# Kernel optimization log

Hardware: AMD Instinct MI355X
Metric: run time of the kernel (lower is better)

The kernel has to match this reference:

```python
import jax, jax.numpy as jnp
import numpy as np

N = 8192
K = 64
EPS = 1e-7
BN_EPS = 1e-5


def _norm(x):
    return jnp.sqrt(jnp.sum(x * x, axis=-1, keepdims=True))


def _bn(x, gamma, beta):
    # BatchNorm2d in training mode (batch statistics, biased variance)
    mu = jnp.mean(x, axis=(0, 2, 3), keepdims=True)
    var = jnp.mean((x - mu) ** 2, axis=(0, 2, 3), keepdims=True)
    return gamma.reshape(1, -1, 1, 1) * (x - mu) / jnp.sqrt(var + BN_EPS) + beta.reshape(1, -1, 1, 1)


def _conv1x1(x, w, b):
    # 1x1 conv == per-pixel linear: x [B,C,H,W], w [O,C]
    return jnp.einsum('bchw,oc->bohw', x, w) + b.reshape(1, -1, 1, 1)


def setup_inputs() -> dict:
    key = jax.random.key(0)
    ks = jax.random.split(key, 24)
    d = {}
    d['points'] = jax.random.normal(ks[0], (1, N, 3), jnp.float32)
    # graph_conv weights (torch code re-draws these every forward; here fixed params)
    lim0 = float(np.sqrt(6.0 / (4 + 64)))
    d['gw0'] = jax.random.uniform(ks[1], (4, 64), jnp.float32, -lim0, lim0)
    lim = float(np.sqrt(6.0 / (64 + 64)))
    for i in range(1, 5):
        d[f'gw{i}'] = jax.random.uniform(ks[1 + i], (64, 64), jnp.float32, -lim, lim)
    # mlp_1: 4->64->128, mlp_2: 192->256->1024 (1x1 convs + BN)
    d['c1w'] = jax.random.normal(ks[6], (64, 4), jnp.float32) * 0.1
    d['c1b'] = jnp.zeros((64,), jnp.float32)
    d['bn1g'] = jnp.ones((64,), jnp.float32)
    d['bn1b'] = jnp.zeros((64,), jnp.float32)
    d['c2w'] = jax.random.normal(ks[7], (128, 64), jnp.float32) * 0.1
    d['c2b'] = jnp.zeros((128,), jnp.float32)
    d['bn2g'] = jnp.ones((128,), jnp.float32)
    d['bn2b'] = jnp.zeros((128,), jnp.float32)
    d['c3w'] = jax.random.normal(ks[8], (256, 192), jnp.float32) * 0.05
    d['c3b'] = jnp.zeros((256,), jnp.float32)
    d['bn3g'] = jnp.ones((256,), jnp.float32)
    d['bn3b'] = jnp.zeros((256,), jnp.float32)
    d['c4w'] = jax.random.normal(ks[9], (1024, 256), jnp.float32) * 0.05
    d['c4b'] = jnp.zeros((1024,), jnp.float32)
    d['bn4g'] = jnp.ones((1024,), jnp.float32)
    d['bn4b'] = jnp.zeros((1024,), jnp.float32)
    return d


def _knn_search(points, k):
    # pairwise squared distances via ||a||^2 - 2ab + ||b||^2
    r = jnp.sum(points * points, axis=-1, keepdims=True)          # [1,N,1]
    dis = r - 2.0 * jnp.einsum('bnd,bmd->bnm', points, points) + jnp.swapaxes(r, 1, 2)
    _, idx = jax.lax.top_k(-dis, k)                                # [1,N,K]
    knn_pts = jax.vmap(lambda p, i: p[i])(points, idx)             # [1,N,K,3]
    return knn_pts


def _proj_knn(knn_pts):
    b, n, k, _ = knn_pts.shape
    pc = knn_pts - knn_pts[:, :, :1, :]                            # center on first neighbor (self)
    vn = jnp.sqrt(jnp.sum(pc * pc, axis=-1))                       # [1,N,K]
    id1 = jnp.argmax(vn, axis=-1)                                  # farthest neighbor
    a1 = jnp.take_along_axis(pc, jnp.broadcast_to(id1[:, :, None, None], (b, n, 1, 3)), axis=2)[:, :, 0, :]
    a1 = a1 / (_norm(a1) + EPS)
    a2 = jnp.mean(pc, axis=2)
    a2 = a2 / (_norm(a2) + EPS)
    a3 = a1 + 1.5 * a2
    a3 = a3 / (_norm(a3) + EPS)
    den = _norm(pc) + EPS                                          # [1,N,K,1]
    f1 = jnp.sum(pc * a1[:, :, None, :], axis=-1, keepdims=True) / den
    f2 = jnp.sum(pc * a2[:, :, None, :], axis=-1, keepdims=True) / den
    f3 = jnp.sum(pc * a3[:, :, None, :], axis=-1, keepdims=True) / den
    return jnp.concatenate([f1, f2, f3, vn[..., None]], axis=-1)   # [1,N,K,4]


def _proj_points(points):
    b, n, _ = points.shape
    vn = jnp.sqrt(jnp.sum(points * points, axis=-1))               # [1,N]
    i1 = jnp.argmax(vn, axis=-1)
    i2 = jnp.argmin(vn, axis=-1)
    a1 = jnp.take_along_axis(points, jnp.broadcast_to(i1[:, None, None], (b, 1, 3)), axis=1)[:, 0, :]
    a1 = a1 / (_norm(a1) + EPS)
    a2 = jnp.take_along_axis(points, jnp.broadcast_to(i2[:, None, None], (b, 1, 3)), axis=1)[:, 0, :]
    a2 = a2 / (_norm(a2) + EPS)
    a3 = a1 + 1.5 * a2
    a3 = a3 / (_norm(a3) + EPS)
    den = _norm(points) + EPS                                      # [1,N,1]
    f1 = jnp.sum(points * a1[:, None, :], axis=-1, keepdims=True) / den
    f2 = jnp.sum(points * a2[:, None, :], axis=-1, keepdims=True) / den
    f3 = jnp.sum(points * a3[:, None, :], axis=-1, keepdims=True) / den
    return jnp.concatenate([f1, f2, f3, vn[..., None]], axis=-1)   # [1,N,4]


def reference(points, gw0, gw1, gw2, gw3, gw4,
              c1w, c1b, bn1g, bn1b, c2w, c2b, bn2g, bn2b,
              c3w, c3b, bn3g, bn3b, c4w, c4b, bn4g, bn4b):
    n = points.shape[1]
    # upper branch: KNN -> rotation-invariant local feats -> 5-layer MLP -> max over K
    knn_pts = _knn_search(points, K)
    feat_up = _proj_knn(knn_pts)                                   # [1,N,K,4]
    x = feat_up.reshape(-1, 4)
    for w in (gw0, gw1, gw2, gw3, gw4):
        x = jax.nn.relu(x @ w)
    x = x.reshape(1, n, K, 64)
    emb_up = jnp.max(x, axis=2, keepdims=True)                     # [1,N,1,64]
    emb_up = emb_up.reshape(1, 64, n, 1)                           # raw view (reshape), as in torch
    # lower branch: global rotation-invariant feats -> mlp_1
    feat_down = _proj_points(points)                               # [1,N,4]
    emb_down = feat_down.reshape(1, 4, n, 1)                       # raw view (reshape), as in torch
    h = jax.nn.relu(_bn(_conv1x1(emb_down, c1w, c1b), bn1g, bn1b))
    h = jax.nn.relu(_bn(_conv1x1(h, c2w, c2b), bn2g, bn2b))        # [1,128,N,1]
    emb = jnp.concatenate([emb_up, h], axis=1)                     # [1,192,N,1]
    out = jax.nn.relu(_bn(_conv1x1(emb, c3w, c3b), bn3g, bn3b))
    out = jax.nn.relu(_bn(_conv1x1(out, c4w, c4b), bn4g, bn4b))    # [1,1024,N,1]
    return out
```

## Files before the change

kernel.cpp:

```cpp
#include <hip/hip_runtime.h>
#include <hip/hip_bf16.h>

#define NPTS 8192
#define KNN 64
#define EPSF 1e-7f

#define OFF_P4      0
#define OFF_STATS   32768
#define OFF_AVEC    36000
#define OFF_PART    36012
#define OFF_FEATDN  36864
#define OFF_WT1     69632
#define OFF_GWT     69888
#define OFF_BW2     79104
#define OFF_BW3     83200
#define OFF_BW4     107776
#define OFF_XB1     238848
#define OFF_XB3     500992
#define OFF_XB4     1287424
#define OFF_Y1      2336000
#define OFF_Y2      2860288
#define OFF_Y3      3908864
#define OFF_FEATUP  6006016

typedef __bf16 bf16x8 __attribute__((ext_vector_type(8)));
typedef float  f32x4  __attribute__((ext_vector_type(4)));

__device__ __forceinline__ unsigned f2u(float f) {
    unsigned u = __float_as_uint(f);
    return ((int)u >= 0) ? (u | 0x80000000u) : ~u;
}
__device__ __forceinline__ float key_to_f(unsigned long long k) {
    unsigned v = (unsigned)(k >> 32);
    unsigned ob = (v & 0x80000000u) ? (v ^ 0x80000000u) : ~v;
    return __uint_as_float(ob);
}
__device__ __forceinline__ unsigned short f2bf(float x) {
    unsigned u = __float_as_uint(x);
    unsigned r = (u + 0x7FFFu + ((u >> 16) & 1u)) >> 16;
    return (unsigned short)r;
}
__device__ __forceinline__ unsigned long long u64min(unsigned long long a, unsigned long long b){ return a < b ? a : b; }
__device__ __forceinline__ unsigned long long u64max(unsigned long long a, unsigned long long b){ return a < b ? b : a; }

__device__ __forceinline__ unsigned long long sort_merge(
    unsigned long long key, unsigned long long cur, int lane)
{
    #pragma unroll
    for (int k = 2; k <= 64; k <<= 1) {
        #pragma unroll
        for (int j = k >> 1; j > 0; j >>= 1) {
            unsigned long long o = __shfl_xor(key, j);
            bool up = ((lane & k) == 0);
            bool lower = ((lane & j) == 0);
            key = (lower == up) ? u64min(key, o) : u64max(key, o);
        }
    }
    unsigned long long rev = __shfl(key, 63 - lane);
    unsigned long long m = u64min(cur, rev);
    #pragma unroll
    for (int j = 32; j > 0; j >>= 1) {
        unsigned long long o = __shfl_xor(m, j);
        m = ((lane & j) == 0) ? u64min(m, o) : u64max(m, o);
    }
    return m;
}

__global__ __launch_bounds__(256) void prep_a_kernel(
    const float* __restrict__ points, float* __restrict__ ws)
{
    const int n = blockIdx.x * 256 + threadIdx.x;
    float x = points[3*n+0], y = points[3*n+1], z = points[3*n+2];
    float rr = x*x + y*y + z*z;
    ((float4*)(ws + OFF_P4))[n] = make_float4(x, y, z, rr);
    float vn = sqrtf(rr);
    unsigned b = __float_as_uint(vn);
    unsigned long long mxk = ((unsigned long long)b << 32) | (unsigned long long)(0xFFFFFFFFu - (unsigned)n);
    unsigned long long mnk = ((unsigned long long)b << 32) | (unsigned long long)(unsigned)n;
    for (int j = 32; j > 0; j >>= 1) {
        mxk = u64max(mxk, __shfl_xor(mxk, j));
        mnk = u64min(mnk, __shfl_xor(mnk, j));
    }
    __shared__ unsigned long long smx[4], smn[4];
    int wid = threadIdx.x >> 6;
    if ((threadIdx.x & 63) == 0) { smx[wid] = mxk; smn[wid] = mnk; }
    __syncthreads();
    if (threadIdx.x == 0) {
        unsigned long long MX = 0ull, MN = ~0ull;
        for (int i = 0; i < 4; ++i) { MX = u64max(MX, smx[i]); MN = u64min(MN, smn[i]); }
        unsigned long long* parts = (unsigned long long*)(ws + OFF_PART);
        parts[2*blockIdx.x + 0] = MX;
        parts[2*blockIdx.x + 1] = MN;
    }
}

__global__ __launch_bounds__(64) void prep_b_kernel(
    const float* __restrict__ points, float* __restrict__ ws)
{
    const int lane = threadIdx.x;
    const unsigned long long* parts = (const unsigned long long*)(ws + OFF_PART);
    unsigned long long mxk = (lane < 32) ? parts[2*lane + 0] : 0ull;
    unsigned long long mnk = (lane < 32) ? parts[2*lane + 1] : ~0ull;
    for (int j = 32; j > 0; j >>= 1) {
        mxk = u64max(mxk, __shfl_xor(mxk, j));
        mnk = u64min(mnk, __shfl_xor(mnk, j));
    }
    if (lane == 0) {
        int i1 = (int)(0xFFFFFFFFu - (unsigned)(mxk & 0xFFFFFFFFu));
        int i2 = (int)(unsigned)(mnk & 0xFFFFFFFFu);
        float a1x = points[3*i1+0], a1y = points[3*i1+1], a1z = points[3*i1+2];
        float n1 = sqrtf(a1x*a1x + a1y*a1y + a1z*a1z) + EPSF;
        a1x /= n1; a1y /= n1; a1z /= n1;
        float a2x = points[3*i2+0], a2y = points[3*i2+1], a2z = points[3*i2+2];
        float n2 = sqrtf(a2x*a2x + a2y*a2y + a2z*a2z) + EPSF;
        a2x /= n2; a2y /= n2; a2z /= n2;
        float a3x = a1x + 1.5f*a2x, a3y = a1y + 1.5f*a2y, a3z = a1z + 1.5f*a2z;
        float n3 = sqrtf(a3x*a3x + a3y*a3y + a3z*a3z) + EPSF;
        a3x /= n3; a3y /= n3; a3z /= n3;
        float* av = ws + OFF_AVEC;
        av[0]=a1x; av[1]=a1y; av[2]=a1z;
        av[3]=a2x; av[4]=a2y; av[5]=a2z;
        av[6]=a3x; av[7]=a3y; av[8]=a3z;
    }
}

__global__ __launch_bounds__(256) void prep_c_kernel(float* __restrict__ ws)
{
    const int n = blockIdx.x * 256 + threadIdx.x;
    const float* av = ws + OFF_AVEC;
    float4 v = ((const float4*)(ws + OFF_P4))[n];
    float vn = sqrtf(v.w);
    float den = vn + EPSF;
    float f1 = (v.x*av[0] + v.y*av[1] + v.z*av[2]) / den;
    float f2 = (v.x*av[3] + v.y*av[4] + v.z*av[5]) / den;
    float f3 = (v.x*av[6] + v.y*av[7] + v.z*av[8]) / den;
    float4* f4 = (float4*)(ws + OFF_FEATDN + 4*n);
    *f4 = make_float4(f1, f2, f3, vn);
}

__global__ __launch_bounds__(256) void wt_kernel(
    const float* __restrict__ c1w, const float* __restrict__ c2w,
    const float* __restrict__ c3w, const float* __restrict__ c4w,
    const float* __restrict__ gw0, const float* __restrict__ gw1,
    const float* __restrict__ gw2, const float* __restrict__ gw3,
    const float* __restrict__ gw4,
    float* __restrict__ ws)
{
    const int t = blockIdx.x * 256 + threadIdx.x;
    const int T = gridDim.x * 256;
    for (int m = t; m < 2944; m += T) ws[OFF_STATS + m] = 0.f;
    for (int m = t; m < 64*4; m += T) { int o = m >> 2, c = m & 3; ws[OFF_WT1 + c*64 + o] = c1w[m]; }

    unsigned short* bw2 = (unsigned short*)(ws + OFF_BW2);
    for (int m = t; m < 128*64; m += T)   bw2[m] = f2bf(c2w[m]);
    unsigned short* bw3 = (unsigned short*)(ws + OFF_BW3);
    for (int m = t; m < 256*192; m += T)  bw3[m] = f2bf(c3w[m]);
    unsigned short* bw4 = (unsigned short*)(ws + OFF_BW4);
    for (int m = t; m < 1024*256; m += T) bw4[m] = f2bf(c4w[m]);

    unsigned short* gwt = (unsigned short*)(ws + OFF_GWT);
    for (int m = t; m < 2048; m += T) {
        int o = m >> 5, i = m & 31;
        gwt[m] = (i < 4) ? f2bf(gw0[i*64 + o]) : (unsigned short)0;
    }
    const float* gsrc[4] = {gw1, gw2, gw3, gw4};
    for (int l = 0; l < 4; ++l) {
        const float* g = gsrc[l];
        unsigned short* dst = gwt + 2048 + l*4096;
        for (int m = t; m < 4096; m += T) { int o = m >> 6, i = m & 63; dst[m] = f2bf(g[i*64 + o]); }
    }
}

__global__ __launch_bounds__(512) void knn_feat_kernel(
    const float4* __restrict__ p4, float4* __restrict__ feat_up)
{
    __shared__ __align__(16) float4 scand[2048];
    __shared__ unsigned long long queue[8][128];
    const int lane = threadIdx.x & 63;
    const int wid  = threadIdx.x >> 6;
    const int q = blockIdx.x * 8 + wid;

    const float4 qa = p4[q];
    unsigned long long cur = ~0ull;
    float kthd = __builtin_inff();
    int qc = 0;
    unsigned long long* Q = queue[wid];

    for (int base = 0; base < NPTS; base += 2048) {
        __syncthreads();
        for (int t = threadIdx.x; t < 2048; t += 512) scand[t] = p4[base + t];
        __syncthreads();
        #pragma unroll 2
        for (int sub = 0; sub < 2048; sub += 64) {
            float4 cd = scand[sub + lane];
            float dot = fmaf(qa.x, cd.x, fmaf(qa.y, cd.y, qa.z * cd.z));
            float d   = fmaf(-2.f, dot, qa.w) + cd.w;
            bool p = d < kthd;
            unsigned long long m = __ballot(p);
            if (m) {
                int prefix = __builtin_amdgcn_mbcnt_hi((unsigned)(m >> 32),
                              __builtin_amdgcn_mbcnt_lo((unsigned)m, 0));
                if (p) Q[qc + prefix] = ((unsigned long long)f2u(d) << 32)
                                      | (unsigned long long)(unsigned)(base + sub + lane);
                qc += __popcll(m);
                if (qc >= 64) {
                    qc -= 64;
                    cur = sort_merge(Q[qc + lane], cur, lane);
                    kthd = key_to_f(__shfl(cur, 63));
                }
            }
        }
    }
    cur = sort_merge((lane < qc) ? Q[lane] : ~0ull, cur, lane);

    int nidx = (int)(unsigned)(cur & 0xFFFFFFFFu);
    float4 np = p4[nidx];
    float ox = __shfl(np.x, 0), oy = __shfl(np.y, 0), oz = __shfl(np.z, 0);
    float pcx = np.x - ox, pcy = np.y - oy, pcz = np.z - oz;
    float vn = sqrtf(pcx*pcx + pcy*pcy + pcz*pcz);

    unsigned long long ak = ((unsigned long long)__float_as_uint(vn) << 32)
                          | (unsigned long long)(unsigned)(63 - lane);
    for (int s = 32; s > 0; s >>= 1) ak = u64max(ak, __shfl_xor(ak, s));
    int id1 = 63 - (int)(unsigned)(ak & 0xFFFFFFFFu);

    float a1x = __shfl(pcx, id1), a1y = __shfl(pcy, id1), a1z = __shfl(pcz, id1);
    float n1 = sqrtf(a1x*a1x + a1y*a1y + a1z*a1z) + EPSF;
    a1x /= n1; a1y /= n1; a1z /= n1;

    float sx = pcx, sy = pcy, sz = pcz;
    for (int s = 32; s > 0; s >>= 1) {
        sx += __shfl_xor(sx, s); sy += __shfl_xor(sy, s); sz += __shfl_xor(sz, s);
    }
    float a2x = sx * (1.f/64.f), a2y = sy * (1.f/64.f), a2z = sz * (1.f/64.f);
    float n2 = sqrtf(a2x*a2x + a2y*a2y + a2z*a2z) + EPSF;
    a2x /= n2; a2y /= n2; a2z /= n2;

    float a3x = a1x + 1.5f*a2x, a3y = a1y + 1.5f*a2y, a3z = a1z + 1.5f*a2z;
    float n3 = sqrtf(a3x*a3x + a3y*a3y + a3z*a3z) + EPSF;
    a3x /= n3; a3y /= n3; a3z /= n3;

    float den = vn + EPSF;
    float f1 = (pcx*a1x + pcy*a1y + pcz*a1z) / den;
    float f2 = (pcx*a2x + pcy*a2y + pcz*a2z) / den;
    float f3 = (pcx*a3x + pcy*a3y + pcz*a3z) / den;
    feat_up[q*64 + lane] = make_float4(f1, f2, f3, vn);
}

#define BROW 72
__global__ __launch_bounds__(256) void mlp_kernel(
    const float4* __restrict__ feat_up,
    const unsigned short* __restrict__ gwt,
    unsigned short* __restrict__ xb3)
{
    __shared__ __align__(16) unsigned short Blds[4][64 * BROW];
    const int lane = threadIdx.x & 63;
    const int wid  = threadIdx.x >> 6;
    const int q = blockIdx.x * 4 + wid;
    const int c = lane & 15, g = lane >> 4;
    unsigned short* B = Blds[wid];

    {
        float4 f = feat_up[q*64 + lane];
        uint2 p0;
        p0.x = (unsigned)f2bf(f.x) | ((unsigned)f2bf(f.y) << 16);
        p0.y = (unsigned)f2bf(f.z) | ((unsigned)f2bf(f.w) << 16);
        *(uint2*)&B[lane*BROW] = p0;
        *(uint2*)&B[lane*BROW + 4] = make_uint2(0, 0);
        uint4 z4 = make_uint4(0, 0, 0, 0);
        *(uint4*)&B[lane*BROW + 8]  = z4;
        *(uint4*)&B[lane*BROW + 16] = z4;
        *(uint4*)&B[lane*BROW + 24] = z4;
    }

    const unsigned short* Wl[5] = {gwt, gwt + 2048, gwt + 6144, gwt + 10240, gwt + 14336};
    f32x4 acc[4][4];

    for (int layer = 0; layer < 5; ++layer) {
        const int wstride = (layer == 0) ? 32 : 64;
        const int nks = (layer == 0) ? 1 : 2;
        #pragma unroll
        for (int mb = 0; mb < 4; ++mb)
            #pragma unroll
            for (int nb = 0; nb < 4; ++nb)
                acc[mb][nb] = (f32x4){0.f, 0.f, 0.f, 0.f};

        for (int ks = 0; ks < nks; ++ks) {
            bf16x8 af[4], bf[4];
            #pragma unroll
            for (int mb = 0; mb < 4; ++mb)
                af[mb] = *(const bf16x8*)(Wl[layer] + (mb*16 + c)*wstride + ks*32 + g*8);
            #pragma unroll
            for (int nb = 0; nb < 4; ++nb)
                bf[nb] = *(const bf16x8*)&B[(nb*16 + c)*BROW + ks*32 + g*8];
            #pragma unroll
            for (int mb = 0; mb < 4; ++mb)
                #pragma unroll
                for (int nb = 0; nb < 4; ++nb)
                    acc[mb][nb] = __builtin_amdgcn_mfma_f32_16x16x32_bf16(af[mb], bf[nb], acc[mb][nb], 0, 0, 0);
        }

        if (layer < 4) {
            #pragma unroll
            for (int mb = 0; mb < 4; ++mb) {
                #pragma unroll
                for (int nb = 0; nb < 4; ++nb) {
                    f32x4 a = acc[mb][nb];
                    float r0 = fmaxf(a[0], 0.f), r1 = fmaxf(a[1], 0.f);
                    float r2 = fmaxf(a[2], 0.f), r3 = fmaxf(a[3], 0.f);
                    uint2 pw;
                    pw.x = (unsigned)f2bf(r0) | ((unsigned)f2bf(r1) << 16);
                    pw.y = (unsigned)f2bf(r2) | ((unsigned)f2bf(r3) << 16);
                    *(uint2*)&B[(nb*16 + c)*BROW + mb*16 + g*4] = pw;
                }
            }
        }
    }

    const int cc = q >> 7;
    const int pbase = (q & 127) << 6;
    #pragma unroll
    for (int mb = 0; mb < 4; ++mb) {
        float v[4];
        #pragma unroll
        for (int r = 0; r < 4; ++r)
            v[r] = fmaxf(fmaxf(fmaxf(acc[mb][0][r], acc[mb][1][r]),
                               fmaxf(acc[mb][2][r], acc[mb][3][r])), 0.f);
        #pragma unroll
        for (int mask = 1; mask <= 8; mask <<= 1)
            #pragma unroll
            for (int r = 0; r < 4; ++r)
                v[r] = fmaxf(v[r], __shfl_xor(v[r], mask));
        if (c == 0) {
            #pragma unroll
            for (int r = 0; r < 4; ++r) {
                const int f = mb*16 + g*4 + r;
                xb3[(size_t)(pbase + f) * 192 + cc] = f2bf(v[r]);
            }
        }
    }
}

__global__ __launch_bounds__(256) void conv1_kernel(
    const float* __restrict__ x, const float* __restrict__ wt,
    const float* __restrict__ bias, float* __restrict__ y,
    float* __restrict__ stout)
{
    const int tid = threadIdx.x;
    const int p  = blockIdx.x * 256 + tid;
    const int o0 = blockIdx.y * 32;
    float acc[32];
    #pragma unroll
    for (int u = 0; u < 32; ++u) acc[u] = bias[o0 + u];
    #pragma unroll
    for (int c = 0; c < 4; ++c) {
        float xv = x[c * NPTS + p];
        const float* wr = wt + c * 64 + o0;
        #pragma unroll
        for (int u = 0; u < 32; ++u) acc[u] = fmaf(xv, wr[u], acc[u]);
    }
    #pragma unroll
    for (int u = 0; u < 32; ++u) y[(o0 + u) * NPTS + p] = acc[u];

    __shared__ float ps[4][32], pss[4][32];
    const int wid = tid >> 6, lane = tid & 63;
    #pragma unroll
    for (int u = 0; u < 32; ++u) {
        float s = acc[u], ss = acc[u] * acc[u];
        for (int j = 32; j > 0; j >>= 1) { s += __shfl_xor(s, j); ss += __shfl_xor(ss, j); }
        if (lane == 0) { ps[wid][u] = s; pss[wid][u] = ss; }
    }
    __syncthreads();
    if (tid < 32) {
        float S  = ps[0][tid] + ps[1][tid] + ps[2][tid] + ps[3][tid];
        float SS = pss[0][tid] + pss[1][tid] + pss[2][tid] + pss[3][tid];
        atomicAdd(&stout[o0 + tid], S);
        atomicAdd(&stout[64 + o0 + tid], SS);
    }
}

__global__ __launch_bounds__(256) void bnpack_kernel(
    const float* __restrict__ y, const float* __restrict__ st,
    const float* __restrict__ gam, const float* __restrict__ bet,
    int C, int stride, int coff, unsigned short* __restrict__ xb)
{
    __shared__ float sc[256], sh[256];
    __shared__ __align__(16) unsigned short tile[64][264];
    const int tid = threadIdx.x;
    for (int cc = tid; cc < C; cc += 256) {
        float mu  = st[cc] * (1.f / 8192.f);
        float var = st[C + cc] * (1.f / 8192.f) - mu * mu;
        float s = gam[cc] / sqrtf(var + 1e-5f);
        sc[cc] = s; sh[cc] = bet[cc] - mu * s;
    }
    __syncthreads();
    const int pl = tid & 63, g = tid >> 6;
    const int p = blockIdx.x * 64 + pl;
    for (int c0 = g * 8; c0 < C; c0 += 32) {
        unsigned pk[4];
        #pragma unroll
        for (int h = 0; h < 4; ++h) {
            float v0 = fmaxf(fmaf(y[(c0 + 2*h    ) * NPTS + p], sc[c0 + 2*h    ], sh[c0 + 2*h    ]), 0.f);
            float v1 = fmaxf(fmaf(y[(c0 + 2*h + 1) * NPTS + p], sc[c0 + 2*h + 1], sh[c0 + 2*h + 1]), 0.f);
            pk[h] = (unsigned)f2bf(v0) | ((unsigned)f2bf(v1) << 16);
        }
        *(uint4*)&tile[pl][c0] = make_uint4(pk[0], pk[1], pk[2], pk[3]);
    }
    __syncthreads();
    const int cpr = C >> 3;
    const int nch = 64 * cpr;
    for (int idx = tid; idx < nch; idx += 256) {
        int r = idx / cpr, cc = (idx - r * cpr) * 8;
        *(uint4*)&xb[(size_t)(blockIdx.x * 64 + r) * stride + coff + cc] = *(uint4*)&tile[r][cc];
    }
}

__global__ __launch_bounds__(256) void conv_mfma_kernel(
    const unsigned short* __restrict__ A, const unsigned short* __restrict__ Bx,
    const float* __restrict__ bias, int K, int M,
    float* __restrict__ y, float* __restrict__ stout)
{
    const int lane = threadIdx.x & 63;
    const int w = threadIdx.x >> 6;
    const int n0 = blockIdx.x * 256 + w * 64;
    const int m0 = blockIdx.y * 64;
    const int c = lane & 15, g = lane >> 4;

    f32x4 acc[4][4];
    #pragma unroll
    for (int mt = 0; mt < 4; ++mt)
        #pragma unroll
        for (int nt = 0; nt < 4; ++nt)
            acc[mt][nt] = (f32x4){0.f, 0.f, 0.f, 0.f};

    for (int k0 = 0; k0 < K; k0 += 32) {
        bf16x8 af[4], bf[4];
        #pragma unroll
        for (int mt = 0; mt < 4; ++mt)
            af[mt] = *(const bf16x8*)(A + (size_t)(m0 + mt*16 + c) * K + k0 + g*8);
        #pragma unroll
        for (int nt = 0; nt < 4; ++nt)
            bf[nt] = *(const bf16x8*)(Bx + (size_t)(n0 + nt*16 + c) * K + k0 + g*8);
        #pragma unroll
        for (int mt = 0; mt < 4; ++mt)
            #pragma unroll
            for (int nt = 0; nt < 4; ++nt)
                acc[mt][nt] = __builtin_amdgcn_mfma_f32_16x16x32_bf16(af[mt], bf[nt], acc[mt][nt], 0, 0, 0);
    }

    #pragma unroll
    for (int mt = 0; mt < 4; ++mt) {
        float s[4], ss[4];
        #pragma unroll
        for (int r = 0; r < 4; ++r) {
            const int o = m0 + mt*16 + g*4 + r;
            const float bv = bias[o];
            float sum = 0.f, sq = 0.f;
            #pragma unroll
            for (int nt = 0; nt < 4; ++nt) {
                float v = acc[mt][nt][r] + bv;
                y[(size_t)o * NPTS + n0 + nt*16 + c] = v;
                sum += v; sq += v * v;
            }
            s[r] = sum; ss[r] = sq;
        }
        #pragma unroll
        for (int mask = 1; mask <= 8; mask <<= 1)
            #pragma unroll
            for (int r = 0; r < 4; ++r) {
                s[r]  += __shfl_xor(s[r],  mask);
                ss[r] += __shfl_xor(ss[r], mask);
            }
        if (c == 0) {
            #pragma unroll
            for (int r = 0; r < 4; ++r) {
                const int o = m0 + mt*16 + g*4 + r;
                atomicAdd(&stout[o], s[r]);
                atomicAdd(&stout[M + o], ss[r]);
            }
        }
    }
}

__global__ __launch_bounds__(256) void bnrelu_kernel(
    const float4* y, const float* __restrict__ st,
    const float* __restrict__ g, const float* __restrict__ b,
    float4* out, int C)
{
    int idx = blockIdx.x * 256 + threadIdx.x;
    int c = idx >> 11;
    float mu  = st[c] * (1.f / 8192.f);
    float var = st[C + c] * (1.f / 8192.f) - mu * mu;
    float scale = g[c] / sqrtf(var + 1e-5f);
    float sh = b[c] - mu * scale;
    float4 v = y[idx];
    v.x = fmaxf(fmaf(v.x, scale, sh), 0.f);
    v.y = fmaxf(fmaf(v.y, scale, sh), 0.f);
    v.z = fmaxf(fmaf(v.z, scale, sh), 0.f);
    v.w = fmaxf(fmaf(v.w, scale, sh), 0.f);
    out[idx] = v;
}

extern "C" void kernel_launch(void* const* d_in, const int* in_sizes, int n_in,
                              void* d_out, int out_size, void* d_ws, size_t ws_size,
                              hipStream_t stream) {
    const float* points = (const float*)d_in[0];
    const float* gw0 = (const float*)d_in[1];
    const float* gw1 = (const float*)d_in[2];
    const float* gw2 = (const float*)d_in[3];
    const float* gw3 = (const float*)d_in[4];
    const float* gw4 = (const float*)d_in[5];
    const float* c1w = (const float*)d_in[6];  const float* c1b = (const float*)d_in[7];
    const float* bn1g = (const float*)d_in[8]; const float* bn1b = (const float*)d_in[9];
    const float* c2w = (const float*)d_in[10]; const float* c2b = (const float*)d_in[11];
    const float* bn2g = (const float*)d_in[12];const float* bn2b = (const float*)d_in[13];
    const float* c3w = (const float*)d_in[14]; const float* c3b = (const float*)d_in[15];
    const float* bn3g = (const float*)d_in[16];const float* bn3b = (const float*)d_in[17];
    const float* c4w = (const float*)d_in[18]; const float* c4b = (const float*)d_in[19];
    const float* bn4g = (const float*)d_in[20];const float* bn4b = (const float*)d_in[21];

    float* ws = (float*)d_ws;
    float* p4f    = ws + OFF_P4;
    float* featdn = ws + OFF_FEATDN;
    float* featup = ws + OFF_FEATUP;
    float* y1 = ws + OFF_Y1; float* y2 = ws + OFF_Y2; float* y3 = ws + OFF_Y3;
    float* s1 = ws + OFF_STATS + 0;
    float* s2 = ws + OFF_STATS + 128;
    float* s3 = ws + OFF_STATS + 384;
    float* s4 = ws + OFF_STATS + 896;
    float* wt1 = ws + OFF_WT1;
    const unsigned short* gwt = (const unsigned short*)(ws + OFF_GWT);
    const unsigned short* bw2 = (const unsigned short*)(ws + OFF_BW2);
    const unsigned short* bw3 = (const unsigned short*)(ws + OFF_BW3);
    const unsigned short* bw4 = (const unsigned short*)(ws + OFF_BW4);
    unsigned short* xb1 = (unsigned short*)(ws + OFF_XB1);
    unsigned short* xb3 = (unsigned short*)(ws + OFF_XB3);
    unsigned short* xb4 = (unsigned short*)(ws + OFF_XB4);
    float* outp = (float*)d_out;

    prep_a_kernel<<<32, 256, 0, stream>>>(points, ws);
    prep_b_kernel<<<1, 64, 0, stream>>>(points, ws);
    prep_c_kernel<<<32, 256, 0, stream>>>(ws);
    wt_kernel<<<256, 256, 0, stream>>>(c1w, c2w, c3w, c4w, gw0, gw1, gw2, gw3, gw4, ws);

    knn_feat_kernel<<<1024, 512, 0, stream>>>((const float4*)p4f, (float4*)featup);
    mlp_kernel<<<2048, 256, 0, stream>>>((const float4*)featup, gwt, xb3);

    conv1_kernel<<<dim3(32, 2), 256, 0, stream>>>(featdn, wt1, c1b, y1, s1);
    bnpack_kernel<<<128, 256, 0, stream>>>(y1, s1, bn1g, bn1b, 64, 64, 0, xb1);
    conv_mfma_kernel<<<dim3(32, 2), 256, 0, stream>>>(bw2, xb1, c2b, 64, 128, y2, s2);
    bnpack_kernel<<<128, 256, 0, stream>>>(y2, s2, bn2g, bn2b, 128, 192, 64, xb3);
    conv_mfma_kernel<<<dim3(32, 4), 256, 0, stream>>>(bw3, xb3, c3b, 192, 256, y3, s3);
    bnpack_kernel<<<128, 256, 0, stream>>>(y3, s3, bn3g, bn3b, 256, 256, 0, xb4);
    conv_mfma_kernel<<<dim3(32, 16), 256, 0, stream>>>(bw4, xb4, c4b, 256, 1024, outp, s4);
    bnrelu_kernel<<<8192, 256, 0, stream>>>((const float4*)outp, s4, bn4g, bn4b, (float4*)outp, 1024);
}
```

Measured before the change: 354.9 us.

## Merge prep kernels, drop constant distance term in KNN, use hardware bf16 convert

Folds the point-prep and weight-conversion kernels into one launch, and moves the axis-vector computation into prep_c so each block recomputes it into shared memory. Two kernel launches go away. The KNN scan now compares ||c||^2 - 2q·c, leaving out the per-query constant ||q||^2, which does not change the ranking. It also processes two 64-candidate groups per iteration to expose more ILP. The f2bf helper now uses a compiler bf16 cast instead of manual rounding, which is equivalent apart from possible NaN handling, and a packing helper is added.

Measured after the change: 350.0 us. No clear change (-1.4%).

```diff
diff --git a/kernel.cpp b/kernel.cpp
--- a/kernel.cpp
+++ b/kernel.cpp
@@ -7,7 +7,6 @@
 
 #define OFF_P4      0
 #define OFF_STATS   32768
-#define OFF_AVEC    36000
 #define OFF_PART    36012
 #define OFF_FEATDN  36864
 #define OFF_WT1     69632
@@ -36,9 +35,12 @@
     return __uint_as_float(ob);
 }
 __device__ __forceinline__ unsigned short f2bf(float x) {
-    unsigned u = __float_as_uint(x);
-    unsigned r = (u + 0x7FFFu + ((u >> 16) & 1u)) >> 16;
-    return (unsigned short)r;
+    union { __bf16 h; unsigned short s; } u;
+    u.h = (__bf16)x;
+    return u.s;
+}
+__device__ __forceinline__ unsigned packbf2(float lo, float hi) {
+    return (unsigned)f2bf(lo) | ((unsigned)f2bf(hi) << 16);
 }
 __device__ __forceinline__ unsigned long long u64min(unsigned long long a, unsigned long long b){ return a < b ? a : b; }
 __device__ __forceinline__ unsigned long long u64max(unsigned long long a, unsigned long long b){ return a < b ? b : a; }
@@ -66,68 +68,97 @@
     return m;
 }
 
-__global__ __launch_bounds__(256) void prep_a_kernel(
-    const float* __restrict__ points, float* __restrict__ ws)
-{
-    const int n = blockIdx.x * 256 + threadIdx.x;
-    float x = points[3*n+0], y = points[3*n+1], z = points[3*n+2];
-    float rr = x*x + y*y + z*z;
-    ((float4*)(ws + OFF_P4))[n] = make_float4(x, y, z, rr);
-    float vn = sqrtf(rr);
-    unsigned b = __float_as_uint(vn);
-    unsigned long long mxk = ((unsigned long long)b << 32) | (unsigned long long)(0xFFFFFFFFu - (unsigned)n);
-    unsigned long long mnk = ((unsigned long long)b << 32) | (unsigned long long)(unsigned)n;
-    for (int j = 32; j > 0; j >>= 1) {
-        mxk = u64max(mxk, __shfl_xor(mxk, j));
-        mnk = u64min(mnk, __shfl_xor(mnk, j));
-    }
-    __shared__ unsigned long long smx[4], smn[4];
-    int wid = threadIdx.x >> 6;
-    if ((threadIdx.x & 63) == 0) { smx[wid] = mxk; smn[wid] = mnk; }
+__global__ __launch_bounds__(256) void prepwt_kernel(
+    const float* __restrict__ points,
+    const float* __restrict__ c1w, const float* __restrict__ c2w,
+    const float* __restrict__ c3w, const float* __restrict__ c4w,
+    const float* __restrict__ gw0, const float* __restrict__ gw1,
+    const float* __restrict__ gw2, const float* __restrict__ gw3,
+    const float* __restrict__ gw4,
+    float* __restrict__ ws)
+{
+    const int t = blockIdx.x * 256 + threadIdx.x;
+    const int T = 256 * 256;
+    for (int m = t; m < 2944; m += T) ws[OFF_STATS + m] = 0.f;
+    for (int m = t; m < 64*4; m += T) { int o = m >> 2, c = m & 3; ws[OFF_WT1 + c*64 + o] = c1w[m]; }
+
+    unsigned short* bw2 = (unsigned short*)(ws + OFF_BW2);
+    for (int m = t; m < 128*64; m += T)   bw2[m] = f2bf(c2w[m]);
+    unsigned short* bw3 = (unsigned short*)(ws + OFF_BW3);
+    for (int m = t; m < 256*192; m += T)  bw3[m] = f2bf(c3w[m]);
+    unsigned short* bw4 = (unsigned short*)(ws + OFF_BW4);
+    for (int m = t; m < 1024*256; m += T) bw4[m] = f2bf(c4w[m]);
+
+    unsigned short* gwt = (unsigned short*)(ws + OFF_GWT);
+    for (int m = t; m < 2048; m += T) {
+        int o = m >> 5, i = m & 31;
+        gwt[m] = (i < 4) ? f2bf(gw0[i*64 + o]) : (unsigned short)0;
+    }
+    const float* gsrc[4] = {gw1, gw2, gw3, gw4};
+    for (int l = 0; l < 4; ++l) {
+        const float* g = gsrc[l];
+        unsigned short* dst = gwt + 2048 + l*4096;
+        for (int m = t; m < 4096; m += T) { int o = m >> 6, i = m & 63; dst[m] = f2bf(g[i*64 + o]); }
+    }
+
+    if (blockIdx.x < 32) {
+        const int n = blockIdx.x * 256 + threadIdx.x;
+        float x = points[3*n+0], y = points[3*n+1], z = points[3*n+2];
+        float rr = x*x + y*y + z*z;
+        ((float4*)(ws + OFF_P4))[n] = make_float4(x, y, z, rr);
+        float vn = sqrtf(rr);
+        unsigned b = __float_as_uint(vn);
+        unsigned long long mxk = ((unsigned long long)b << 32) | (unsigned long long)(0xFFFFFFFFu - (unsigned)n);
+        unsigned long long mnk = ((unsigned long long)b << 32) | (unsigned long long)(unsigned)n;
+        for (int j = 32; j > 0; j >>= 1) {
+            mxk = u64max(mxk, __shfl_xor(mxk, j));
+            mnk = u64min(mnk, __shfl_xor(mnk, j));
+        }
+        __shared__ unsigned long long smx[4], smn[4];
+        int wid = threadIdx.x >> 6;
+        if ((threadIdx.x & 63) == 0) { smx[wid] = mxk; smn[wid] = mnk; }
+        __syncthreads();
+        if (threadIdx.x == 0) {
+            unsigned long long MX = 0ull, MN = ~0ull;
+            for (int i = 0; i < 4; ++i) { MX = u64max(MX, smx[i]); MN = u64min(MN, smn[i]); }
+            unsigned long long* parts = (unsigned long long*)(ws + OFF_PART);
+            parts[2*blockIdx.x + 0] = MX;
+            parts[2*blockIdx.x + 1] = MN;
+        }
+    }
+}
+
+__global__ __launch_bounds__(256) void prep_c_kernel(float* __restrict__ ws)
+{
+    __shared__ float av[9];
+    const int tid = threadIdx.x;
+    if (tid < 64) {
+        const unsigned long long* parts = (const unsigned long long*)(ws + OFF_PART);
+        unsigned long long mxk = (tid < 32) ? parts[2*tid + 0] : 0ull;
+        unsigned long long mnk = (tid < 32) ? parts[2*tid + 1] : ~0ull;
+        for (int j = 32; j > 0; j >>= 1) {
+            mxk = u64max(mxk, __shfl_xor(mxk, j));
+            mnk = u64min(mnk, __shfl_xor(mnk, j));
+        }
+        if (tid == 0) {
+            int i1 = (int)(0xFFFFFFFFu - (unsigned)(mxk & 0xFFFFFFFFu));
+            int i2 = (int)(unsigned)(mnk & 0xFFFFFFFFu);
+            float4 p1 = ((const float4*)(ws + OFF_P4))[i1];
+            float4 p2 = ((const float4*)(ws + OFF_P4))[i2];
+            float n1 = sqrtf(p1.x*p1.x + p1.y*p1.y + p1.z*p1.z) + EPSF;
+            float a1x = p1.x/n1, a1y = p1.y/n1, a1z = p1.z/n1;
+            float n2 = sqrtf(p2.x*p2.x + p2.y*p2.y + p2.z*p2.z) + EPSF;
+            float a2x = p2.x/n2, a2y = p2.y/n2, a2z = p2.z/n2;
+            float a3x = a1x + 1.5f*a2x, a3y = a1y + 1.5f*a2y, a3z = a1z + 1.5f*a2z;
+            float n3 = sqrtf(a3x*a3x + a3y*a3y + a3z*a3z) + EPSF;
+            a3x /= n3; a3y /= n3; a3z /= n3;
+            av[0]=a1x; av[1]=a1y; av[2]=a1z;
+            av[3]=a2x; av[4]=a2y; av[5]=a2z;
+            av[6]=a3x; av[7]=a3y; av[8]=a3z;
+        }
+    }
     __syncthreads();
-    if (threadIdx.x == 0) {
-        unsigned long long MX = 0ull, MN = ~0ull;
-        for (int i = 0; i < 4; ++i) { MX = u64max(MX, smx[i]); MN = u64min(MN, smn[i]); }
-        unsigned long long* parts = (unsigned long long*)(ws + OFF_PART);
-        parts[2*blockIdx.x + 0] = MX;
-        parts[2*blockIdx.x + 1] = MN;
-    }
-}
-
-__global__ __launch_bounds__(64) void prep_b_kernel(
-    const float* __restrict__ points, float* __restrict__ ws)
-{
-    const int lane = threadIdx.x;
-    const unsigned long long* parts = (const unsigned long long*)(ws + OFF_PART);
-    unsigned long long mxk = (lane < 32) ? parts[2*lane + 0] : 0ull;
-    unsigned long long mnk = (lane < 32) ? parts[2*lane + 1] : ~0ull;
-    for (int j = 32; j > 0; j >>= 1) {
-        mxk = u64max(mxk, __shfl_xor(mxk, j));
-        mnk = u64min(mnk, __shfl_xor(mnk, j));
-    }
-    if (lane == 0) {
-        int i1 = (int)(0xFFFFFFFFu - (unsigned)(mxk & 0xFFFFFFFFu));
-        int i2 = (int)(unsigned)(mnk & 0xFFFFFFFFu);
-        float a1x = points[3*i1+0], a1y = points[3*i1+1], a1z = points[3*i1+2];
-        float n1 = sqrtf(a1x*a1x + a1y*a1y + a1z*a1z) + EPSF;
-        a1x /= n1; a1y /= n1; a1z /= n1;
-        float a2x = points[3*i2+0], a2y = points[3*i2+1], a2z = points[3*i2+2];
-        float n2 = sqrtf(a2x*a2x + a2y*a2y + a2z*a2z) + EPSF;
-        a2x /= n2; a2y /= n2; a2z /= n2;
-        float a3x = a1x + 1.5f*a2x, a3y = a1y + 1.5f*a2y, a3z = a1z + 1.5f*a2z;
-        float n3 = sqrtf(a3x*a3x + a3y*a3y + a3z*a3z) + EPSF;
-        a3x /= n3; a3y /= n3; a3z /= n3;
-        float* av = ws + OFF_AVEC;
-        av[0]=a1x; av[1]=a1y; av[2]=a1z;
-        av[3]=a2x; av[4]=a2y; av[5]=a2z;
-        av[6]=a3x; av[7]=a3y; av[8]=a3z;
-    }
-}
-
-__global__ __launch_bounds__(256) void prep_c_kernel(float* __restrict__ ws)
-{
-    const int n = blockIdx.x * 256 + threadIdx.x;
-    const float* av = ws + OFF_AVEC;
+    const int n = blockIdx.x * 256 + tid;
     float4 v = ((const float4*)(ws + OFF_P4))[n];
     float vn = sqrtf(v.w);
     float den = vn + EPSF;
@@ -138,39 +169,6 @@
     *f4 = make_float4(f1, f2, f3, vn);
 }
 
-__global__ __launch_bounds__(256) void wt_kernel(
-    const float* __restrict__ c1w, const float* __restrict__ c2w,
-    const float* __restrict__ c3w, const float* __restrict__ c4w,
-    const float* __restrict__ gw0, const float* __restrict__ gw1,
-    const float* __restrict__ gw2, const float* __restrict__ gw3,
-    const float* __restrict__ gw4,
-    float* __restrict__ ws)
-{
-    const int t = blockIdx.x * 256 + threadIdx.x;
-    const int T = gridDim.x * 256;
-    for (int m = t; m < 2944; m += T) ws[OFF_STATS + m] = 0.f;
-    for (int m = t; m < 64*4; m += T) { int o = m >> 2, c = m & 3; ws[OFF_WT1 + c*64 + o] = c1w[m]; }
-
-    unsigned short* bw2 = (unsigned short*)(ws + OFF_BW2);
-    for (int m = t; m < 128*64; m += T)   bw2[m] = f2bf(c2w[m]);
-    unsigned short* bw3 = (unsigned short*)(ws + OFF_BW3);
-    for (int m = t; m < 256*192; m += T)  bw3[m] = f2bf(c3w[m]);
-    unsigned short* bw4 = (unsigned short*)(ws + OFF_BW4);
-    for (int m = t; m < 1024*256; m += T) bw4[m] = f2bf(c4w[m]);
-
-    unsigned short* gwt = (unsigned short*)(ws + OFF_GWT);
-    for (int m = t; m < 2048; m += T) {
-        int o = m >> 5, i = m & 31;
-        gwt[m] = (i < 4) ? f2bf(gw0[i*64 + o]) : (unsigned short)0;
-    }
-    const float* gsrc[4] = {gw1, gw2, gw3, gw4};
-    for (int l = 0; l < 4; ++l) {
-        const float* g = gsrc[l];
-        unsigned short* dst = gwt + 2048 + l*4096;
-        for (int m = t; m < 4096; m += T) { int o = m >> 6, i = m & 63; dst[m] = f2bf(g[i*64 + o]); }
-    }
-}
-
 __global__ __launch_bounds__(512) void knn_feat_kernel(
     const float4* __restrict__ p4, float4* __restrict__ feat_up)
 {
@@ -182,7 +180,7 @@
 
     const float4 qa = p4[q];
     unsigned long long cur = ~0ull;
-    float kthd = __builtin_inff();
+    float ke = __builtin_inff();
     int qc = 0;
     unsigned long long* Q = queue[wid];
 
@@ -191,22 +189,39 @@
         for (int t = threadIdx.x; t < 2048; t += 512) scand[t] = p4[base + t];
         __syncthreads();
         #pragma unroll 2
-        for (int sub = 0; sub < 2048; sub += 64) {
-            float4 cd = scand[sub + lane];
-            float dot = fmaf(qa.x, cd.x, fmaf(qa.y, cd.y, qa.z * cd.z));
-            float d   = fmaf(-2.f, dot, qa.w) + cd.w;
-            bool p = d < kthd;
-            unsigned long long m = __ballot(p);
-            if (m) {
-                int prefix = __builtin_amdgcn_mbcnt_hi((unsigned)(m >> 32),
-                              __builtin_amdgcn_mbcnt_lo((unsigned)m, 0));
-                if (p) Q[qc + prefix] = ((unsigned long long)f2u(d) << 32)
-                                      | (unsigned long long)(unsigned)(base + sub + lane);
-                qc += __popcll(m);
+        for (int sub = 0; sub < 2048; sub += 128) {
+            float4 cd0 = scand[sub + lane];
+            float4 cd1 = scand[sub + 64 + lane];
+            float dot0 = fmaf(qa.x, cd0.x, fmaf(qa.y, cd0.y, qa.z * cd0.z));
+            float dot1 = fmaf(qa.x, cd1.x, fmaf(qa.y, cd1.y, qa.z * cd1.z));
+            float e0 = fmaf(-2.f, dot0, cd0.w);
+            float e1 = fmaf(-2.f, dot1, cd1.w);
+            bool p0 = e0 < ke;
+            bool p1 = e1 < ke;
+            unsigned long long m0 = __ballot(p0);
+            unsigned long long m1 = __ballot(p1);
+            if (m0) {
+                int prefix = __builtin_amdgcn_mbcnt_hi((unsigned)(m0 >> 32),
+                              __builtin_amdgcn_mbcnt_lo((unsigned)m0, 0));
+                if (p0) Q[qc + prefix] = ((unsigned long long)f2u(e0) << 32)
+                                       | (unsigned long long)(unsigned)(base + sub + lane);
+                qc += __popcll(m0);
                 if (qc >= 64) {
                     qc -= 64;
                     cur = sort_merge(Q[qc + lane], cur, lane);
-                    kthd = key_to_f(__shfl(cur, 63));
+                    ke = key_to_f(__shfl(cur, 63));
+                }
+            }
+            if (m1) {
+                int prefix = __builtin_amdgcn_mbcnt_hi((unsigned)(m1 >> 32),
+                              __builtin_amdgcn_mbcnt_lo((unsigned)m1, 0));
+                if (p1) Q[qc + prefix] = ((unsigned long long)f2u(e1) << 32)
+                                       | (unsigned long long)(unsigned)(base + sub + 64 + lane);
+                qc += __popcll(m1);
+                if (qc >= 64) {
+                    qc -= 64;
+                    cur = sort_merge(Q[qc + lane], cur, lane);
+                    ke = key_to_f(__shfl(cur, 63));
                 }
             }
         }
@@ -263,8 +278,8 @@
     {
         float4 f = feat_up[q*64 + lane];
         uint2 p0;
-        p0.x = (unsigned)f2bf(f.x) | ((unsigned)f2bf(f.y) << 16);
-        p0.y = (unsigned)f2bf(f.z) | ((unsigned)f2bf(f.w) << 16);
+        p0.x = packbf2(f.x, f.y);
+        p0.y = packbf2(f.z, f.w);
         *(uint2*)&B[lane*BROW] = p0;
         *(uint2*)&B[lane*BROW + 4] = make_uint2(0, 0);
         uint4 z4 = make_uint4(0, 0, 0, 0);
@@ -306,11 +321,9 @@
                 #pragma unroll
                 for (int nb = 0; nb < 4; ++nb) {
                     f32x4 a = acc[mb][nb];
-                    float r0 = fmaxf(a[0], 0.f), r1 = fmaxf(a[1], 0.f);
-                    float r2 = fmaxf(a[2], 0.f), r3 = fmaxf(a[3], 0.f);
                     uint2 pw;
-                    pw.x = (unsigned)f2bf(r0) | ((unsigned)f2bf(r1) << 16);
-                    pw.y = (unsigned)f2bf(r2) | ((unsigned)f2bf(r3) << 16);
+                    pw.x = packbf2(fmaxf(a[0], 0.f), fmaxf(a[1], 0.f));
+                    pw.y = packbf2(fmaxf(a[2], 0.f), fmaxf(a[3], 0.f));
                     *(uint2*)&B[(nb*16 + c)*BROW + mb*16 + g*4] = pw;
                 }
             }
@@ -402,7 +415,7 @@
         for (int h = 0; h < 4; ++h) {
             float v0 = fmaxf(fmaf(y[(c0 + 2*h    ) * NPTS + p], sc[c0 + 2*h    ], sh[c0 + 2*h    ]), 0.f);
             float v1 = fmaxf(fmaf(y[(c0 + 2*h + 1) * NPTS + p], sc[c0 + 2*h + 1], sh[c0 + 2*h + 1]), 0.f);
-            pk[h] = (unsigned)f2bf(v0) | ((unsigned)f2bf(v1) << 16);
+            pk[h] = packbf2(v0, v1);
         }
         *(uint4*)&tile[pl][c0] = make_uint4(pk[0], pk[1], pk[2], pk[3]);
     }
@@ -538,10 +551,9 @@
     unsigned short* xb4 = (unsigned short*)(ws + OFF_XB4);
     float* outp = (float*)d_out;
 
-    prep_a_kernel<<<32, 256, 0, stream>>>(points, ws);
-    prep_b_kernel<<<1, 64, 0, stream>>>(points, ws);
+    prepwt_kernel<<<256, 256, 0, stream>>>(points, c1w, c2w, c3w, c4w,
+                                           gw0, gw1, gw2, gw3, gw4, ws);
     prep_c_kernel<<<32, 256, 0, stream>>>(ws);
-    wt_kernel<<<256, 256, 0, stream>>>(c1w, c2w, c3w, c4w, gw0, gw1, gw2, gw3, gw4, ws);
 
     knn_feat_kernel<<<1024, 512, 0, stream>>>((const float4*)p4f, (float4*)featup);
     mlp_kernel<<<2048, 256, 0, stream>>>((const float4*)featup, gwt, xb3);
```
